# Kernel optimization log

Measured on AMD Instinct MI355X. Metric: run time of the kernel, lower is better.

## Reference

```python
import jax, jax.numpy as jnp
import numpy as np
from jax import lax

EPSILON = 1e-12


def _sobel_kernels(n1=1, n2=2, n3=2):
    Sx = np.asarray([[[-n1, 0, n1], [-n2, 0, n2], [-n1, 0, n1]],
                     [[-n2, 0, n2], [-n3 * n2, 0, n3 * n2], [-n2, 0, n2]],
                     [[-n1, 0, n1], [-n2, 0, n2], [-n1, 0, n1]]])
    Sy = np.asarray([[[-n1, -n2, -n1], [0, 0, 0], [n1, n2, n1]],
                     [[-n2, -n3 * n2, -n2], [0, 0, 0], [n2, n3 * n2, n2]],
                     [[-n1, -n2, -n1], [0, 0, 0], [n1, n2, n1]]])
    Sz = np.asarray([[[-n1, -n2, -n1], [-n2, -n3 * n2, -n2], [-n1, -n2, -n1]],
                     [[0, 0, 0], [0, 0, 0], [0, 0, 0]],
                     [[n1, n2, n1], [n2, n3 * n2, n2], [n1, n2, n1]]])
    Sd11 = np.asarray([[[0, n1, n2], [-n1, 0, n1], [-n2, -n1, 0]],
                       [[0, n2, n2 * n3], [-n2, 0, n2], [-n2 * n3, -n2, 0]],
                       [[0, n1, n2], [-n1, 0, n1], [-n2, -n1, 0]]])
    Sd12 = np.asarray([[[-n2, -n1, 0], [-n1, 0, n1], [0, n1, n2]],
                       [[-n2 * n3, -n2, 0], [-n2, 0, n2], [0, n2, n2 * n3]],
                       [[-n2, -n1, 0], [-n1, 0, n1], [0, n1, n2]]])
    Sd21 = Sd11.T
    Sd22 = Sd12.T
    Sd31 = np.asarray([-S.T for S in Sd11.T])
    Sd32 = np.asarray([S.T for S in Sd12.T])
    ks = np.stack([Sx, Sy, Sz, Sd11, Sd12, Sd21, Sd22, Sd31, Sd32]).astype(np.float32)
    return jnp.asarray(ks[:, None])  # [9, 1, 3, 3, 3] (OIDHW)


_KERNELS = _sobel_kernels(1, 2, 2)


def _edge_magnitude(img):
    # img: [B, C, H, W, D]. Per-channel convs are summed over C in the original;
    # by linearity of conv, sum channels first, then run all 9 stencils at once.
    C = img.shape[1]
    x = jnp.sum(img, axis=1, keepdims=True)  # [B, 1, H, W, D]
    g = lax.conv_general_dilated(
        x, _KERNELS, window_strides=(1, 1, 1), padding='SAME',
        dimension_numbers=('NCDHW', 'OIDHW', 'NCDHW'))  # [B, 9, H, W, D]
    mag = jnp.sqrt(jnp.sum(g * g, axis=1, keepdims=True) + EPSILON)
    return mag / C  # (1/C) * sqrt(sum_sq + eps), matches operator precedence


def setup_inputs() -> dict:
    key = jax.random.key(0)
    k1, k2 = jax.random.split(key)
    shape = (2, 2, 128, 128, 128)
    y = jax.random.normal(k1, shape, dtype=jnp.float32)
    yp = jax.random.normal(k2, shape, dtype=jnp.float32)
    return {"y": y, "yp": yp}


def reference(y, yp):
    y_edge = _edge_magnitude(y)
    yp_edge = _edge_magnitude(yp)
    return jnp.mean((y_edge - yp_edge) ** 2)  # nn.MSELoss default 'mean'
```

## Files before the change

### kernel.cpp

```cpp
#include <hip/hip_runtime.h>


namespace {

constexpr int ZDIM = 128, YDIM = 128, XDIM = 128;
constexpr int TX = 32, TY = 8, ZC = 8;
constexpr int LW = 40;
constexpr int ROWS = TY + 2;
constexpr int PLANE = ROWS * LW;
constexpr int QPR = LW / 4;
constexpr int NSLOT = ROWS * QPR;
constexpr int YX = YDIM * XDIM;
constexpr size_t CS = (size_t)ZDIM * YX;
constexpr float INV_N = 1.0f / 4194304.0f;

__device__ __forceinline__ void plane_combos(const float* __restrict__ p,
                                             float* __restrict__ C) {
  float sx[3], dx[3], ex[3];
#pragma unroll
  for (int r = 0; r < 3; ++r) {
    const float a0 = p[r * LW + 0];
    const float a1 = p[r * LW + 1];
    const float a2 = p[r * LW + 2];
    const float t = a0 + a2;
    ex[r] = t + a1;
    sx[r] = __builtin_fmaf(2.0f, a1, t);
    dx[r] = a2 - a0;
  }
  C[3] = (dx[0] + dx[2]) + dx[1];
  C[0] = C[3] + dx[1];
  C[1] = sx[2] - sx[0];
  C[5] = (sx[0] + sx[2]) + sx[1];
  C[2] = C[5] + sx[1];
  C[4] = ex[2] - ex[0];
  C[6] = __builtin_fmaf(2.0f, ex[1], ex[0] + ex[2]);
}

__device__ __forceinline__ float edge_mag_half(const float* __restrict__ Ca,
                                               const float* __restrict__ Cb,
                                               const float* __restrict__ Cc) {
  const float g1  = __builtin_fmaf(2.0f, Cb[0], Ca[0] + Cc[0]);
  const float g2  = __builtin_fmaf(2.0f, Cb[1], Ca[1] + Cc[1]);
  const float g3  = Cc[2] - Ca[2];
  const float Azx = __builtin_fmaf(2.0f, Cb[3], Ca[3] + Cc[3]);
  const float Azy = __builtin_fmaf(2.0f, Cb[4], Ca[4] + Cc[4]);
  const float Axz = Cc[5] - Ca[5];
  const float Axy = g2 - Cb[1];
  const float Ayx = g1 - Cb[0];
  const float Ayz = Cc[6] - Ca[6];
  const float g4 = Azx - Azy, g5 = Azx + Azy;
  const float g6 = Axz - Axy, g7 = Axz + Axy;
  const float g8 = Ayx - Ayz, g9 = Ayx + Ayz;
  float s = __builtin_fmaf(g1, g1, 1e-12f);
  s = __builtin_fmaf(g2, g2, s); s = __builtin_fmaf(g3, g3, s);
  s = __builtin_fmaf(g4, g4, s); s = __builtin_fmaf(g5, g5, s);
  s = __builtin_fmaf(g6, g6, s); s = __builtin_fmaf(g7, g7, s);
  s = __builtin_fmaf(g8, g8, s); s = __builtin_fmaf(g9, g9, s);
  return 0.5f * sqrtf(s);
}

__global__ __launch_bounds__(256, 4)
void gme_loss_kernel(const float* __restrict__ y,
                     const float* __restrict__ yp,
                     float* __restrict__ out) {
  const int tx  = threadIdx.x;
  const int ty  = threadIdx.y;
  const int tid = ty * TX + tx;

  const int bx = blockIdx.x;
  const int x0 = (bx & 3) * TX;
  const int y0 = (bx >> 2) * TY;
  const int z0 = blockIdx.y * ZC;
  const int b  = blockIdx.z;

  __shared__ __align__(16) float lds[2][2][PLANE];
  __shared__ float red[4];

  const bool has_slot = tid < 2 * NSLOT;
  bool sok = false;
  const float* gp = nullptr;
  float* w0 = nullptr; float* w1 = nullptr;
  if (has_slot) {
    const int vol = tid >= NSLOT;
    const int s   = tid - vol * NSLOT;
    const int ly  = s / QPR;
    const int lx  = s - ly * QPR;
    const int py  = y0 - 1 + ly;
    const int px  = x0 - 4 + 4 * lx;
    sok = (py >= 0) & (py < YDIM) & (px >= 0) & (px <= XDIM - 4);
    const float* src = vol ? yp : y;
    gp = src + (size_t)b * 2 * CS + (size_t)py * XDIM + px;
    w0 = &lds[vol][0][ly * LW + lx * 4];
    w1 = &lds[vol][1][ly * LW + lx * 4];
  }

  const int ridx = ty * LW + tx + 3;
  const float* rY0 = &lds[0][0][ridx];
  const float* rY1 = &lds[0][1][ridx];
  const float* rP0 = &lds[1][0][ridx];
  const float* rP1 = &lds[1][1][ridx];

  auto prefetch = [&](int zc) -> float4 {
    float4 v = make_float4(0.f, 0.f, 0.f, 0.f);
    if (sok && (unsigned)zc < (unsigned)ZDIM) {
      const float* p = gp + (size_t)zc * YX;
      const float4 a = *(const float4*)p;
      const float4 c = *(const float4*)(p + CS);
      v.x = a.x + c.x; v.y = a.y + c.y; v.z = a.z + c.z; v.w = a.w + c.w;
    }
    return v;
  };

  float KY[3][7] = {}, KP[3][7] = {};
  float acc = 0.0f;

  float4 pf = prefetch(z0 - 1);

#pragma unroll
  for (int i = 0; i < ZC + 2; ++i) {
    const int zc = z0 - 1 + i;
    if (has_slot) {
      float* w = (i & 1) ? w1 : w0;
      *(float4*)w = pf;
    }
    if (i < ZC + 1) pf = prefetch(zc + 1);
    __syncthreads();

    float* Cc_y = KY[i % 3];
    float* Cc_p = KP[i % 3];
    plane_combos((i & 1) ? rY1 : rY0, Cc_y);
    plane_combos((i & 1) ? rP1 : rP0, Cc_p);

    if (i >= 2) {
      const float* Ca_y = KY[(i + 1) % 3];
      const float* Cb_y = KY[(i + 2) % 3];
      const float* Ca_p = KP[(i + 1) % 3];
      const float* Cb_p = KP[(i + 2) % 3];
      const float my = edge_mag_half(Ca_y, Cb_y, Cc_y);
      const float mp = edge_mag_half(Ca_p, Cb_p, Cc_p);
      const float d = my - mp;
      acc = __builtin_fmaf(d, d, acc);
    }
  }

#pragma unroll
  for (int off = 32; off > 0; off >>= 1) acc += __shfl_down(acc, off);
  const int lane = tid & 63;
  const int wave = tid >> 6;
  if (lane == 0) red[wave] = acc;
  __syncthreads();
  if (tid == 0) {
    const float s = (red[0] + red[1] + red[2] + red[3]) * INV_N;
    atomicAdd(out, s);
  }
}

}

extern "C" void kernel_launch(void* const* d_in, const int* in_sizes, int n_in,
                              void* d_out, int out_size, void* d_ws, size_t ws_size,
                              hipStream_t stream) {
  const float* y  = (const float*)d_in[0];
  const float* yp = (const float*)d_in[1];
  float* out = (float*)d_out;

  hipMemsetAsync(out, 0, sizeof(float), stream);

  dim3 block(TX, TY, 1);
  dim3 grid((XDIM / TX) * (YDIM / TY),
            ZDIM / ZC,
            2);
  gme_loss_kernel<<<grid, block, 0, stream>>>(y, yp, out);
}
```

Before: 128.5 us.

## Replace LDS-tiled stencil with wave-per-row direct loads and shuffle halos

Drops the shared-memory plane tiles and block barriers. Each 64-lane wave now owns one y-row segment across 16 z-planes and loads the three neighbouring rows straight from global memory. X-direction neighbours are exchanged with wave shuffles, and edge lanes fetch halo values separately. This is meant to remove LDS traffic and __syncthreads, but it reloads each y-row three times from global/L2, and the halo loads in edge lanes diverge from the rest of the wave.

Result: slower. 159.9 us (+24.4%).

```diff
diff --git a/kernel.cpp b/kernel.cpp
--- a/kernel.cpp
+++ b/kernel.cpp
@@ -3,38 +3,10 @@
 
 namespace {
 
-constexpr int ZDIM = 128, YDIM = 128, XDIM = 128;
-constexpr int TX = 32, TY = 8, ZC = 8;
-constexpr int LW = 40;
-constexpr int ROWS = TY + 2;
-constexpr int PLANE = ROWS * LW;
-constexpr int QPR = LW / 4;
-constexpr int NSLOT = ROWS * QPR;
-constexpr int YX = YDIM * XDIM;
-constexpr size_t CS = (size_t)ZDIM * YX;
+constexpr int YX = 128 * 128;
+constexpr ptrdiff_t CS = (ptrdiff_t)128 * YX;
+constexpr int ZC = 16;
 constexpr float INV_N = 1.0f / 4194304.0f;
-
-__device__ __forceinline__ void plane_combos(const float* __restrict__ p,
-                                             float* __restrict__ C) {
-  float sx[3], dx[3], ex[3];
-#pragma unroll
-  for (int r = 0; r < 3; ++r) {
-    const float a0 = p[r * LW + 0];
-    const float a1 = p[r * LW + 1];
-    const float a2 = p[r * LW + 2];
-    const float t = a0 + a2;
-    ex[r] = t + a1;
-    sx[r] = __builtin_fmaf(2.0f, a1, t);
-    dx[r] = a2 - a0;
-  }
-  C[3] = (dx[0] + dx[2]) + dx[1];
-  C[0] = C[3] + dx[1];
-  C[1] = sx[2] - sx[0];
-  C[5] = (sx[0] + sx[2]) + sx[1];
-  C[2] = C[5] + sx[1];
-  C[4] = ex[2] - ex[0];
-  C[6] = __builtin_fmaf(2.0f, ex[1], ex[0] + ex[2]);
-}
 
 __device__ __forceinline__ float edge_mag_half(const float* __restrict__ Ca,
                                                const float* __restrict__ Cb,
@@ -59,100 +31,121 @@
   return 0.5f * sqrtf(s);
 }
 
-__global__ __launch_bounds__(256, 4)
+__device__ __forceinline__ void combos7(const float* __restrict__ s,
+                                        const float* __restrict__ h,
+                                        bool l0, bool l63, int seg,
+                                        float* __restrict__ C) {
+  const float t  = s[0] + s[2];
+  const float ys = __builtin_fmaf(2.0f, s[1], t);
+  const float ye = t + s[1];
+  const float yd = s[2] - s[0];
+  const float th  = h[0] + h[2];
+  const float hys = __builtin_fmaf(2.0f, h[1], th);
+  const float hye = th + h[1];
+  const float hyd = h[2] - h[0];
+  float ysL = __shfl_up(ys, 1),  ydL = __shfl_up(yd, 1),  yeL = __shfl_up(ye, 1);
+  float ysR = __shfl_down(ys, 1), ydR = __shfl_down(yd, 1), yeR = __shfl_down(ye, 1);
+  const float eLs = seg ? hys : 0.0f, eLd = seg ? hyd : 0.0f, eLe = seg ? hye : 0.0f;
+  const float eRs = seg ? 0.0f : hys, eRd = seg ? 0.0f : hyd, eRe = seg ? 0.0f : hye;
+  ysL = l0 ? eLs : ysL;  ydL = l0 ? eLd : ydL;  yeL = l0 ? eLe : yeL;
+  ysR = l63 ? eRs : ysR; ydR = l63 ? eRd : ydR; yeR = l63 ? eRe : yeR;
+  C[0] = ysR - ysL;
+  const float tds = ydL + ydR;
+  C[1] = __builtin_fmaf(2.0f, yd, tds);
+  C[4] = tds + yd;
+  const float tss = ysL + ysR;
+  C[2] = __builtin_fmaf(2.0f, ys, tss);
+  C[6] = tss + ys;
+  C[3] = yeR - yeL;
+  const float tes = yeL + yeR;
+  C[5] = __builtin_fmaf(2.0f, ye, tes);
+}
+
+__global__ __launch_bounds__(64)
 void gme_loss_kernel(const float* __restrict__ y,
                      const float* __restrict__ yp,
                      float* __restrict__ out) {
-  const int tx  = threadIdx.x;
-  const int ty  = threadIdx.y;
-  const int tid = ty * TX + tx;
+  const int lane = threadIdx.x;
+  const int yy   = blockIdx.x;
+  const int seg  = blockIdx.y >> 3;
+  const int z0   = (blockIdx.y & 7) * ZC;
+  const int b    = blockIdx.z;
+  const int px   = seg * 64 + lane;
+  const bool l0 = (lane == 0), l63 = (lane == 63);
+  const bool isEdge = seg ? l0 : l63;
+  const ptrdiff_t hd = seg ? -1 : 1;
+  const float w0 = (yy > 0)   ? 1.0f : 0.0f;
+  const float w2 = (yy < 127) ? 1.0f : 0.0f;
+  const int r0 = (yy > 0) ? yy - 1 : 0;
+  const int r2 = (yy < 127) ? yy + 1 : 127;
 
-  const int bx = blockIdx.x;
-  const int x0 = (bx & 3) * TX;
-  const int y0 = (bx >> 2) * TY;
-  const int z0 = blockIdx.y * ZC;
-  const int b  = blockIdx.z;
+  const float* Yb = y  + (ptrdiff_t)b * 2 * CS;
+  const float* Pb = yp + (ptrdiff_t)b * 2 * CS;
+  const ptrdiff_t o0 = (ptrdiff_t)r0 * 128 + px;
+  const ptrdiff_t o1 = (ptrdiff_t)yy * 128 + px;
+  const ptrdiff_t o2 = (ptrdiff_t)r2 * 128 + px;
 
-  __shared__ __align__(16) float lds[2][2][PLANE];
-  __shared__ float red[4];
+  float ar[12];
+  float hr[12];
+#pragma unroll
+  for (int j = 0; j < 12; ++j) { ar[j] = 0.0f; hr[j] = 0.0f; }
 
-  const bool has_slot = tid < 2 * NSLOT;
-  bool sok = false;
-  const float* gp = nullptr;
-  float* w0 = nullptr; float* w1 = nullptr;
-  if (has_slot) {
-    const int vol = tid >= NSLOT;
-    const int s   = tid - vol * NSLOT;
-    const int ly  = s / QPR;
-    const int lx  = s - ly * QPR;
-    const int py  = y0 - 1 + ly;
-    const int px  = x0 - 4 + 4 * lx;
-    sok = (py >= 0) & (py < YDIM) & (px >= 0) & (px <= XDIM - 4);
-    const float* src = vol ? yp : y;
-    gp = src + (size_t)b * 2 * CS + (size_t)py * XDIM + px;
-    w0 = &lds[vol][0][ly * LW + lx * 4];
-    w1 = &lds[vol][1][ly * LW + lx * 4];
-  }
+  float sY[3], hY[3], sP[3], hP[3];
 
-  const int ridx = ty * LW + tx + 3;
-  const float* rY0 = &lds[0][0][ridx];
-  const float* rY1 = &lds[0][1][ridx];
-  const float* rP0 = &lds[1][0][ridx];
-  const float* rP1 = &lds[1][1][ridx];
-
-  auto prefetch = [&](int zc) -> float4 {
-    float4 v = make_float4(0.f, 0.f, 0.f, 0.f);
-    if (sok && (unsigned)zc < (unsigned)ZDIM) {
-      const float* p = gp + (size_t)zc * YX;
-      const float4 a = *(const float4*)p;
-      const float4 c = *(const float4*)(p + CS);
-      v.x = a.x + c.x; v.y = a.y + c.y; v.z = a.z + c.z; v.w = a.w + c.w;
+  auto issue = [&](int zl) {
+    if ((unsigned)zl < 128u) {
+      const float* Yz = Yb + (ptrdiff_t)zl * YX;
+      const float* Pz = Pb + (ptrdiff_t)zl * YX;
+      ar[0] = Yz[o0]; ar[1]  = Yz[o0 + CS];
+      ar[2] = Yz[o1]; ar[3]  = Yz[o1 + CS];
+      ar[4] = Yz[o2]; ar[5]  = Yz[o2 + CS];
+      ar[6] = Pz[o0]; ar[7]  = Pz[o0 + CS];
+      ar[8] = Pz[o1]; ar[9]  = Pz[o1 + CS];
+      ar[10] = Pz[o2]; ar[11] = Pz[o2 + CS];
+      if (isEdge) {
+        hr[0] = Yz[o0 + hd]; hr[1]  = Yz[o0 + CS + hd];
+        hr[2] = Yz[o1 + hd]; hr[3]  = Yz[o1 + CS + hd];
+        hr[4] = Yz[o2 + hd]; hr[5]  = Yz[o2 + CS + hd];
+        hr[6] = Pz[o0 + hd]; hr[7]  = Pz[o0 + CS + hd];
+        hr[8] = Pz[o1 + hd]; hr[9]  = Pz[o1 + CS + hd];
+        hr[10] = Pz[o2 + hd]; hr[11] = Pz[o2 + CS + hd];
+      }
+    } else {
+#pragma unroll
+      for (int j = 0; j < 12; ++j) { ar[j] = 0.0f; hr[j] = 0.0f; }
     }
-    return v;
+  };
+  auto reduceb = [&]() {
+    sY[0] = (ar[0] + ar[1]) * w0;  sY[1] = ar[2] + ar[3];  sY[2] = (ar[4] + ar[5]) * w2;
+    sP[0] = (ar[6] + ar[7]) * w0;  sP[1] = ar[8] + ar[9];  sP[2] = (ar[10] + ar[11]) * w2;
+    hY[0] = (hr[0] + hr[1]) * w0;  hY[1] = hr[2] + hr[3];  hY[2] = (hr[4] + hr[5]) * w2;
+    hP[0] = (hr[6] + hr[7]) * w0;  hP[1] = hr[8] + hr[9];  hP[2] = (hr[10] + hr[11]) * w2;
   };
 
-  float KY[3][7] = {}, KP[3][7] = {};
+  float KY[3][7], KP[3][7];
   float acc = 0.0f;
 
-  float4 pf = prefetch(z0 - 1);
+  issue(z0 - 1);
+  reduceb();
 
-#pragma unroll
+#pragma unroll 6
   for (int i = 0; i < ZC + 2; ++i) {
-    const int zc = z0 - 1 + i;
-    if (has_slot) {
-      float* w = (i & 1) ? w1 : w0;
-      *(float4*)w = pf;
-    }
-    if (i < ZC + 1) pf = prefetch(zc + 1);
-    __syncthreads();
-
-    float* Cc_y = KY[i % 3];
-    float* Cc_p = KP[i % 3];
-    plane_combos((i & 1) ? rY1 : rY0, Cc_y);
-    plane_combos((i & 1) ? rP1 : rP0, Cc_p);
-
+    const int zl = (i < ZC + 1) ? (z0 + i) : 128;
+    issue(zl);
+    combos7(sY, hY, l0, l63, seg, KY[i % 3]);
+    combos7(sP, hP, l0, l63, seg, KP[i % 3]);
     if (i >= 2) {
-      const float* Ca_y = KY[(i + 1) % 3];
-      const float* Cb_y = KY[(i + 2) % 3];
-      const float* Ca_p = KP[(i + 1) % 3];
-      const float* Cb_p = KP[(i + 2) % 3];
-      const float my = edge_mag_half(Ca_y, Cb_y, Cc_y);
-      const float mp = edge_mag_half(Ca_p, Cb_p, Cc_p);
+      const float my = edge_mag_half(KY[(i + 1) % 3], KY[(i + 2) % 3], KY[i % 3]);
+      const float mp = edge_mag_half(KP[(i + 1) % 3], KP[(i + 2) % 3], KP[i % 3]);
       const float d = my - mp;
       acc = __builtin_fmaf(d, d, acc);
     }
+    reduceb();
   }
 
 #pragma unroll
   for (int off = 32; off > 0; off >>= 1) acc += __shfl_down(acc, off);
-  const int lane = tid & 63;
-  const int wave = tid >> 6;
-  if (lane == 0) red[wave] = acc;
-  __syncthreads();
-  if (tid == 0) {
-    const float s = (red[0] + red[1] + red[2] + red[3]) * INV_N;
-    atomicAdd(out, s);
-  }
+  if (lane == 0) atomicAdd(out, acc * INV_N);
 }
 
 }
@@ -166,9 +159,9 @@
 
   hipMemsetAsync(out, 0, sizeof(float), stream);
 
-  dim3 block(TX, TY, 1);
-  dim3 grid((XDIM / TX) * (YDIM / TY),
-            ZDIM / ZC,
+  dim3 block(64, 1, 1);
+  dim3 grid(128,
+            16,
             2);
   gme_loss_kernel<<<grid, block, 0, stream>>>(y, yp, out);
 }
```
